# Kernel tuning notes

Hardware: AMD Instinct MI355X
Metric: run time of the kernel (lower is better)

Reference implementation:

```python
import jax, jax.numpy as jnp
import numpy as np

N = 50000      # nodes
E = 800000     # unique directed edges (avg degree 16)
F = 64         # input_dim
D = 64         # output_dim (== F -> residual is identity)
ALPHA = 0.5
LCS_THR = 0.5  # enable_lcs_masking=True, lcs_threshold=0.5


def setup_inputs() -> dict:
    key = jax.random.key(0)
    ks = jax.random.split(key, 16)
    x = jax.random.normal(ks[0], (N, F), jnp.float32)
    src = jax.random.randint(ks[1], (E,), 0, N, jnp.int32)
    dst = jax.random.randint(ks[2], (E,), 0, N, jnp.int32)
    # integer-valued multiplicities in {1,2,3,4} (recurring-transaction counts)
    counts = jnp.floor(jax.random.uniform(ks[3], (E,), jnp.float32) * 4.0) + 1.0
    def lin(k, fan_in, shape):
        return jax.random.normal(k, shape, jnp.float32) / np.float32(np.sqrt(fan_in))
    return dict(
        x=x, counts=counts,
        W_s2d=lin(ks[4], F, (F, D)), b_s2d=jnp.zeros((D,), jnp.float32),
        W_d2s=lin(ks[5], F, (F, D)), b_d2s=jnp.zeros((D,), jnp.float32),
        W_l1=lin(ks[6], 2 * F, (2 * F, F)), b_l1=jnp.zeros((F,), jnp.float32),
        W_l2=lin(ks[7], F, (F, 1)), b_l2=jnp.zeros((1,), jnp.float32),
        W_g1=lin(ks[8], 2 * D, (2 * D, D)), b_g1=jnp.zeros((D,), jnp.float32),
        W_g2=lin(ks[9], D, (D, 1)), b_g2=jnp.zeros((1,), jnp.float32),
        src=src, dst=dst,
    )


def reference(x, counts, W_s2d, b_s2d, W_d2s, b_d2s,
              W_l1, b_l1, W_l2, b_l2, W_g1, b_g1, W_g2, b_g2,
              src, dst):
    # in/out degrees from full (unmasked) multiplicities, clamped at 1
    in_deg = jnp.maximum(jax.ops.segment_sum(counts, dst, num_segments=N), 1.0)
    out_deg = jnp.maximum(jax.ops.segment_sum(counts, src, num_segments=N), 1.0)

    # LCS per unique edge: sigmoid(MLP([x_src, x_dst])), detached in torch
    lcs_in = jnp.concatenate([x[src], x[dst]], axis=-1)          # [E, 2F]
    lcs = jax.nn.sigmoid(
        jax.nn.relu(lcs_in @ W_l1 + b_l1) @ W_l2 + b_l2)[:, 0]   # [E]
    lcs = jax.lax.stop_gradient(lcs)
    keep = (lcs >= LCS_THR).astype(x.dtype)                      # LCS masking

    # symmetric-normalized edge weights with multiplicity counts
    w = counts * keep * jax.lax.rsqrt(out_deg[src] * in_deg[dst])  # [E]

    # direction-aware message passing (redundancy-eliminated, per unique edge)
    h_s2d = x @ W_s2d + b_s2d                                    # [N, D]
    h_d2s = x @ W_d2s + b_d2s                                    # [N, D]
    m_in = jax.ops.segment_sum(w[:, None] * h_s2d[src], dst, num_segments=N)
    m_out = jax.ops.segment_sum(w[:, None] * h_d2s[dst], src, num_segments=N)

    # node-wise gating over inbound vs outbound flows
    gate = jax.nn.sigmoid(
        jax.nn.relu(jnp.concatenate([m_in, m_out], axis=-1) @ W_g1 + b_g1)
        @ W_g2 + b_g2)                                           # [N, 1]

    # gated alpha-blend + identity residual (input_dim == output_dim)
    out = ALPHA * gate * m_in + (1.0 - ALPHA) * (1.0 - gate) * m_out + x
    return out
```

## Files before the change

kernel.cpp:

```cpp
#include <hip/hip_runtime.h>
#include <math.h>


typedef unsigned long long u64;
typedef unsigned short u16;

__device__ __forceinline__ float bflo(unsigned u) { return __uint_as_float(u << 16); }
__device__ __forceinline__ float bfhi(unsigned u) { return __uint_as_float(u & 0xffff0000u); }
__device__ __forceinline__ unsigned rne16(float f) {
    unsigned u = __float_as_uint(f);
    return (u + 0x7fffu + ((u >> 16) & 1u)) >> 16;
}

__global__ __launch_bounds__(256) void proj_zero_kernel(
    const float* __restrict__ x,
    const float* __restrict__ Wl1,  const float* __restrict__ bl1,
    const float* __restrict__ Ws2d, const float* __restrict__ bs2d,
    const float* __restrict__ Wd2s, const float* __restrict__ bd2s,
    float* __restrict__ A, float* __restrict__ B,
    unsigned* __restrict__ Ah, unsigned* __restrict__ Bh,
    unsigned* __restrict__ HSh, unsigned* __restrict__ HDh,
    int* __restrict__ zp, int nzero, int PB, int N)
{
    if (blockIdx.x >= PB) {
        const int t0 = (blockIdx.x - PB) * 256 + threadIdx.x;
        const int stride = (gridDim.x - PB) * 256;
        for (int i = t0; i < nzero; i += stride) zp[i] = 0;
        return;
    }
    __shared__ float xs[64][64];
    const int tid = threadIdx.x;
    const int n0  = blockIdx.x * 64;
    const int wv  = tid >> 6;
    const int cc  = tid & 63;

    const float* Wbase; const float* bias; float* obase; unsigned* obh;
    switch (wv) {
        case 0:  Wbase = Wl1;           bias = bl1;     obase = A;       obh = Ah;  break;
        case 1:  Wbase = Wl1 + 64 * 64; bias = nullptr; obase = B;       obh = Bh;  break;
        case 2:  Wbase = Ws2d;          bias = bs2d;    obase = nullptr; obh = HSh; break;
        default: Wbase = Wd2s;          bias = bd2s;    obase = nullptr; obh = HDh; break;
    }

    float wr[64];
#pragma unroll
    for (int k = 0; k < 64; ++k) wr[k] = Wbase[k * 64 + cc];
    const float bv = bias ? bias[cc] : 0.f;

#pragma unroll
    for (int j = 0; j < 4; ++j) {
        int f4  = tid + j * 256;
        int row = f4 >> 4;
        int c4  = f4 & 15;
        int gn  = n0 + row;
        float4 v = (gn < N) ? ((const float4*)x)[(long)gn * 16 + c4]
                            : make_float4(0.f, 0.f, 0.f, 0.f);
        ((float4*)&xs[row][0])[c4] = v;
    }
    __syncthreads();

    const int nmax = (N - n0 < 64) ? (N - n0) : 64;
    for (int n = 0; n < nmax; ++n) {
        float acc = bv;
#pragma unroll
        for (int k = 0; k < 64; k += 4) {
            float4 xv = *((const float4*)&xs[n][k]);
            acc += xv.x * wr[k] + xv.y * wr[k + 1] + xv.z * wr[k + 2] + xv.w * wr[k + 3];
        }
        if (obase) obase[(long)(n0 + n) * 64 + cc] = acc;
        const float part = __shfl_xor(acc, 1);
        if ((cc & 1) == 0)
            obh[(long)(n0 + n) * 32 + (cc >> 1)] = (rne16(part) << 16) | rne16(acc);
    }
}

#define LCS_MARGIN 0.04f
__global__ __launch_bounds__(256) void edge_w_kernel(
    const int* __restrict__ src, const int* __restrict__ dst,
    const float* __restrict__ counts,
    const float* __restrict__ A, const float* __restrict__ B,
    const unsigned* __restrict__ Ah, const unsigned* __restrict__ Bh,
    const float* __restrict__ Wl2, const float* __restrict__ bl2,
    u64* __restrict__ pk, unsigned* __restrict__ kslot, int N, int E)
{
    const int tid = threadIdx.x;
    const int e   = blockIdx.x * 16 + (tid >> 4);
    const int c   = tid & 15;
    if (e >= E) return;

    const int s = src[e];
    const int d = dst[e];
    const uint2 ua = *((const uint2*)(Ah + (long)s * 32 + c * 2));
    const uint2 ub = *((const uint2*)(Bh + (long)d * 32 + c * 2));
    const float4 wl = *((const float4*)(Wl2 + c * 4));

    float p = fmaxf(bflo(ua.x) + bflo(ub.x), 0.f) * wl.x
            + fmaxf(bfhi(ua.x) + bfhi(ub.x), 0.f) * wl.y
            + fmaxf(bflo(ua.y) + bflo(ub.y), 0.f) * wl.z
            + fmaxf(bfhi(ua.y) + bfhi(ub.y), 0.f) * wl.w;
    p += __shfl_xor(p, 1); p += __shfl_xor(p, 2);
    p += __shfl_xor(p, 4); p += __shfl_xor(p, 8);

    float z = p + bl2[0];
    if (fabsf(z) < LCS_MARGIN) {
        const float4 a = *((const float4*)(A + (long)s * 64 + c * 4));
        const float4 b = *((const float4*)(B + (long)d * 64 + c * 4));
        float q = fmaxf(a.x + b.x, 0.f) * wl.x + fmaxf(a.y + b.y, 0.f) * wl.y
                + fmaxf(a.z + b.z, 0.f) * wl.z + fmaxf(a.w + b.w, 0.f) * wl.w;
        q += __shfl_xor(q, 1); q += __shfl_xor(q, 2);
        q += __shfl_xor(q, 4); q += __shfl_xor(q, 8);
        z = q + bl2[0];
    }

    if (c == 0) {
        const u64 keep = (z >= 0.f) ? 1ull : 0ull;
        const u64 ic = (u64)(unsigned)__float2int_rn(counts[e]);
        const u64 od = atomicAdd(pk + d,     (keep << 32) | ic);
        const u64 os = atomicAdd(pk + N + s, (keep << 32) | ic);
        kslot[e] = keep ? ((((unsigned)(os >> 32)) << 16) | (unsigned)(od >> 32))
                        : 0xFFFFFFFFu;
    }
}

__global__ __launch_bounds__(256) void scan_reduce_kernel(
    const u64* __restrict__ pk, int* __restrict__ bsum, int M)
{
    __shared__ int sh[256];
    const int idx = blockIdx.x * 256 + threadIdx.x;
    sh[threadIdx.x] = (idx < M) ? (int)(pk[idx] >> 32) : 0;
    __syncthreads();
#pragma unroll
    for (int off = 128; off > 0; off >>= 1) {
        if (threadIdx.x < off) sh[threadIdx.x] += sh[threadIdx.x + off];
        __syncthreads();
    }
    if (threadIdx.x == 0) bsum[blockIdx.x] = sh[0];
}

__global__ __launch_bounds__(256) void scan_write_kernel(
    const u64* __restrict__ pk, const int* __restrict__ bsum,
    int* __restrict__ rp, int2* __restrict__ pkd, int2* __restrict__ pks,
    int M , int N, int NCH)
{
    __shared__ int s0[512], s1[512];
    const int tid = threadIdx.x;

    s0[tid]       = (tid < NCH)       ? bsum[tid]       : 0;
    s0[tid + 256] = (tid + 256 < NCH) ? bsum[tid + 256] : 0;
    __syncthreads();
    {
        int* cur = s0; int* nxt = s1;
        for (int off = 1; off < 512; off <<= 1) {
            nxt[tid]       = cur[tid]       + ((tid >= off)       ? cur[tid - off]       : 0);
            nxt[tid + 256] = cur[tid + 256] + ((tid + 256 >= off) ? cur[tid + 256 - off] : 0);
            __syncthreads();
            int* t = cur; cur = nxt; nxt = t;
        }
        if (tid == 0) s1[511] = 0;
        __syncthreads();
        if (cur != s0) { s0[tid] = cur[tid]; s0[tid + 256] = cur[tid + 256]; __syncthreads(); }
    }
    const int boff = (blockIdx.x == 0) ? 0 : s0[blockIdx.x - 1];
    __syncthreads();

    const int idx = blockIdx.x * 256 + tid;
    const u64 pv  = (idx < M) ? pk[idx] : 0ull;
    const int v   = (int)(pv >> 32);
    s0[tid] = v;
    __syncthreads();
    {
        int* cur = s0; int* nxt = s1;
        for (int off = 1; off < 256; off <<= 1) {
            nxt[tid] = cur[tid] + ((tid >= off) ? cur[tid - off] : 0);
            __syncthreads();
            int* t = cur; cur = nxt; nxt = t;
        }
        if (idx < M) {
            const int base = cur[tid] - v + boff;
            rp[idx] = base;
            const float isq = 1.f / sqrtf(fmaxf((float)(unsigned)pv, 1.f));
            if (idx < N) pkd[idx]     = make_int2(base, __float_as_int(isq));
            else         pks[idx - N] = make_int2(base, __float_as_int(isq));
            if (idx == M - 1) rp[M] = base + v;
        }
    }
}

__global__ __launch_bounds__(256) void place_kernel(
    const int* __restrict__ src, const int* __restrict__ dst,
    const float* __restrict__ counts, const unsigned* __restrict__ kslot,
    const int2* __restrict__ pkd, const int2* __restrict__ pks,
    unsigned* __restrict__ rec, int E)
{
    const int e = blockIdx.x * 256 + threadIdx.x;
    if (e >= E) return;
    const unsigned kk = kslot[e];
    if (kk == 0xFFFFFFFFu) return;
    const int s = src[e];
    const int d = dst[e];
    const int2 qd = pkd[d];
    const int2 qs = pks[s];
    const float w = counts[e] * __int_as_float(qd.y) * __int_as_float(qs.y);
    const unsigned wb = rne16(w);
    rec[qd.x + (int)(kk & 0xFFFFu)] = ((unsigned)s << 16) | wb;
    rec[qs.x + (int)(kk >> 16)]     = ((unsigned)d << 16) | wb;
}

__global__ __launch_bounds__(256) void gather_gate_kernel(
    const int* __restrict__ rp, const unsigned* __restrict__ rec,
    const unsigned* __restrict__ HSh, const unsigned* __restrict__ HDh,
    const float* __restrict__ x,
    const float* __restrict__ Wg1, const float* __restrict__ bg1,
    const float* __restrict__ Wg2, const float* __restrict__ bg2,
    float* __restrict__ out, int N)
{
    __shared__ float mbuf[4][128];
    const int tid  = threadIdx.x;
    const int wv   = tid >> 6;
    const int lane = tid & 63;
    const int g    = lane >> 3;
    const int c    = lane & 7;
    const int n    = blockIdx.x * 4 + wv;
    if (n >= N) return;

    float mi[8], mo[8];
#pragma unroll
    for (int j = 0; j < 8; ++j) { mi[j] = 0.f; mo[j] = 0.f; }

    {
        const int end = rp[n + 1];
        int i = rp[n] + g;
        for (; i + 8 < end; i += 16) {
            const unsigned ra = rec[i];
            const unsigned rb = rec[i + 8];
            const float wa = bflo(ra), wb = bflo(rb);
            const uint4 ua = *((const uint4*)(HSh + (long)(ra >> 16) * 32 + c * 4));
            const uint4 ub = *((const uint4*)(HSh + (long)(rb >> 16) * 32 + c * 4));
            mi[0] += wa * bflo(ua.x) + wb * bflo(ub.x);
            mi[1] += wa * bfhi(ua.x) + wb * bfhi(ub.x);
            mi[2] += wa * bflo(ua.y) + wb * bflo(ub.y);
            mi[3] += wa * bfhi(ua.y) + wb * bfhi(ub.y);
            mi[4] += wa * bflo(ua.z) + wb * bflo(ub.z);
            mi[5] += wa * bfhi(ua.z) + wb * bfhi(ub.z);
            mi[6] += wa * bflo(ua.w) + wb * bflo(ub.w);
            mi[7] += wa * bfhi(ua.w) + wb * bfhi(ub.w);
        }
        if (i < end) {
            const unsigned ra = rec[i];
            const float wa = bflo(ra);
            const uint4 ua = *((const uint4*)(HSh + (long)(ra >> 16) * 32 + c * 4));
            mi[0] += wa * bflo(ua.x); mi[1] += wa * bfhi(ua.x);
            mi[2] += wa * bflo(ua.y); mi[3] += wa * bfhi(ua.y);
            mi[4] += wa * bflo(ua.z); mi[5] += wa * bfhi(ua.z);
            mi[6] += wa * bflo(ua.w); mi[7] += wa * bfhi(ua.w);
        }
    }
    {
        const int end = rp[N + n + 1];
        int i = rp[N + n] + g;
        for (; i + 8 < end; i += 16) {
            const unsigned ra = rec[i];
            const unsigned rb = rec[i + 8];
            const float wa = bflo(ra), wb = bflo(rb);
            const uint4 ua = *((const uint4*)(HDh + (long)(ra >> 16) * 32 + c * 4));
            const uint4 ub = *((const uint4*)(HDh + (long)(rb >> 16) * 32 + c * 4));
            mo[0] += wa * bflo(ua.x) + wb * bflo(ub.x);
            mo[1] += wa * bfhi(ua.x) + wb * bfhi(ub.x);
            mo[2] += wa * bflo(ua.y) + wb * bflo(ub.y);
            mo[3] += wa * bfhi(ua.y) + wb * bfhi(ub.y);
            mo[4] += wa * bflo(ua.z) + wb * bflo(ub.z);
            mo[5] += wa * bfhi(ua.z) + wb * bfhi(ub.z);
            mo[6] += wa * bflo(ua.w) + wb * bflo(ub.w);
            mo[7] += wa * bfhi(ua.w) + wb * bfhi(ub.w);
        }
        if (i < end) {
            const unsigned ra = rec[i];
            const float wa = bflo(ra);
            const uint4 ua = *((const uint4*)(HDh + (long)(ra >> 16) * 32 + c * 4));
            mo[0] += wa * bflo(ua.x); mo[1] += wa * bfhi(ua.x);
            mo[2] += wa * bflo(ua.y); mo[3] += wa * bfhi(ua.y);
            mo[4] += wa * bflo(ua.z); mo[5] += wa * bfhi(ua.z);
            mo[6] += wa * bflo(ua.w); mo[7] += wa * bfhi(ua.w);
        }
    }

#pragma unroll
    for (int j = 0; j < 8; ++j) {
        mi[j] += __shfl_xor(mi[j], 8);
        mi[j] += __shfl_xor(mi[j], 16);
        mi[j] += __shfl_xor(mi[j], 32);
        mo[j] += __shfl_xor(mo[j], 8);
        mo[j] += __shfl_xor(mo[j], 16);
        mo[j] += __shfl_xor(mo[j], 32);
    }
    if (g == 0) {
#pragma unroll
        for (int j = 0; j < 8; ++j) {
            mbuf[wv][c * 8 + j]      = mi[j];
            mbuf[wv][64 + c * 8 + j] = mo[j];
        }
    }

    float acc = bg1[lane];
    const float* mb = &mbuf[wv][0];
#pragma unroll 8
    for (int k4 = 0; k4 < 32; ++k4) {
        const float4 m4 = ((const float4*)mb)[k4];
        const int k = k4 * 4;
        acc += m4.x * Wg1[(k + 0) * 64 + lane] + m4.y * Wg1[(k + 1) * 64 + lane]
             + m4.z * Wg1[(k + 2) * 64 + lane] + m4.w * Wg1[(k + 3) * 64 + lane];
    }
    float v = fmaxf(acc, 0.f) * Wg2[lane];
    v += __shfl_xor(v, 1);  v += __shfl_xor(v, 2);  v += __shfl_xor(v, 4);
    v += __shfl_xor(v, 8);  v += __shfl_xor(v, 16); v += __shfl_xor(v, 32);

    const float gate = 1.f / (1.f + expf(-(v + bg2[0])));
    const float miv = mb[lane];
    const float mov = mb[64 + lane];
    out[(long)n * 64 + lane] = 0.5f * gate * miv + 0.5f * (1.f - gate) * mov
                             + x[(long)n * 64 + lane];
}

extern "C" void kernel_launch(void* const* d_in, const int* in_sizes, int n_in,
                              void* d_out, int out_size, void* d_ws, size_t ws_size,
                              hipStream_t stream) {
    const float* x      = (const float*)d_in[0];
    const float* counts = (const float*)d_in[1];
    const float* Ws2d   = (const float*)d_in[2];
    const float* bs2d   = (const float*)d_in[3];
    const float* Wd2s   = (const float*)d_in[4];
    const float* bd2s   = (const float*)d_in[5];
    const float* Wl1    = (const float*)d_in[6];
    const float* bl1    = (const float*)d_in[7];
    const float* Wl2    = (const float*)d_in[8];
    const float* bl2    = (const float*)d_in[9];
    const float* Wg1    = (const float*)d_in[10];
    const float* bg1    = (const float*)d_in[11];
    const float* Wg2    = (const float*)d_in[12];
    const float* bg2    = (const float*)d_in[13];
    const int*   src    = (const int*)d_in[14];
    const int*   dst    = (const int*)d_in[15];

    const int N   = in_sizes[0] / 64;
    const int E   = in_sizes[14];
    const int M   = 2 * N;
    const int NCH = (M + 255) / 256;
    const int PB  = (N + 63) / 64;

    float* ws      = (float*)d_ws;
    float* A       = ws;
    float* B       = A + 64L * N;
    unsigned* Ah   = (unsigned*)(B + 64L * N);
    unsigned* Bh   = Ah + 32L * N;
    unsigned* HSh  = Bh + 32L * N;
    unsigned* HDh  = HSh + 32L * N;
    u64* pk        = (u64*)(HDh + 32L * N);
    int* bsum      = (int*)(pk + M);
    int* rp        = bsum + 512;
    int2* pkd      = (int2*)(rp + M + 2);
    int2* pks      = pkd + N;
    unsigned* kslot = (unsigned*)(pks + N);
    unsigned* rec   = kslot + (long)E;

    proj_zero_kernel<<<PB + 64, 256, 0, stream>>>(
        x, Wl1, bl1, Ws2d, bs2d, Wd2s, bd2s, A, B, Ah, Bh, HSh, HDh,
        (int*)pk, 4 * N, PB, N);

    edge_w_kernel<<<(E + 15) / 16, 256, 0, stream>>>(
        src, dst, counts, A, B, Ah, Bh, Wl2, bl2, pk, kslot, N, E);

    scan_reduce_kernel<<<NCH, 256, 0, stream>>>(pk, bsum, M);

    scan_write_kernel<<<NCH, 256, 0, stream>>>(pk, bsum, rp, pkd, pks, M, N, NCH);

    place_kernel<<<(E + 255) / 256, 256, 0, stream>>>(
        src, dst, counts, kslot, pkd, pks, rec, E);

    gather_gate_kernel<<<(N + 3) / 4, 256, 0, stream>>>(
        rp, rec, HSh, HDh, x, Wg1, bg1, Wg2, bg2, (float*)d_out, N);
}
```

Baseline: 293.4 us.

## Widen edge LCS loads to 8 lanes per edge and repack gate weights as float4

The edge scoring kernel now uses 8 lanes per edge with 16-byte loads instead of 16 lanes with 8-byte loads. That halves the shuffle reduction steps and doubles the edges handled per block. An extra block in the projection kernel rearranges Wg1 into a float4-interleaved layout, so the gate MLP in the gather kernel issues one vector load per four weights. An unneeded shared-memory write and barrier in the scan are also removed. The cost is an extra workspace region that shifts every other buffer, plus a small extra block in the first launch.

```diff
diff --git a/kernel.cpp b/kernel.cpp
--- a/kernel.cpp
+++ b/kernel.cpp
@@ -17,14 +17,22 @@
     const float* __restrict__ Wl1,  const float* __restrict__ bl1,
     const float* __restrict__ Ws2d, const float* __restrict__ bs2d,
     const float* __restrict__ Wd2s, const float* __restrict__ bd2s,
+    const float* __restrict__ Wg1,  float* __restrict__ Wg1q,
     float* __restrict__ A, float* __restrict__ B,
     unsigned* __restrict__ Ah, unsigned* __restrict__ Bh,
     unsigned* __restrict__ HSh, unsigned* __restrict__ HDh,
     int* __restrict__ zp, int nzero, int PB, int N)
 {
     if (blockIdx.x >= PB) {
+        if (blockIdx.x == PB + 64) {
+            for (int i = threadIdx.x; i < 8192; i += 256) {
+                const int k = i >> 6, c = i & 63;
+                Wg1q[((k >> 2) * 64 + c) * 4 + (k & 3)] = Wg1[i];
+            }
+            return;
+        }
         const int t0 = (blockIdx.x - PB) * 256 + threadIdx.x;
-        const int stride = (gridDim.x - PB) * 256;
+        const int stride = 64 * 256;
         for (int i = t0; i < nzero; i += stride) zp[i] = 0;
         return;
     }
@@ -84,31 +92,38 @@
     u64* __restrict__ pk, unsigned* __restrict__ kslot, int N, int E)
 {
     const int tid = threadIdx.x;
-    const int e   = blockIdx.x * 16 + (tid >> 4);
-    const int c   = tid & 15;
+    const int e   = blockIdx.x * 32 + (tid >> 3);
+    const int c   = tid & 7;
     if (e >= E) return;
 
     const int s = src[e];
     const int d = dst[e];
-    const uint2 ua = *((const uint2*)(Ah + (long)s * 32 + c * 2));
-    const uint2 ub = *((const uint2*)(Bh + (long)d * 32 + c * 2));
-    const float4 wl = *((const float4*)(Wl2 + c * 4));
-
-    float p = fmaxf(bflo(ua.x) + bflo(ub.x), 0.f) * wl.x
-            + fmaxf(bfhi(ua.x) + bfhi(ub.x), 0.f) * wl.y
-            + fmaxf(bflo(ua.y) + bflo(ub.y), 0.f) * wl.z
-            + fmaxf(bfhi(ua.y) + bfhi(ub.y), 0.f) * wl.w;
-    p += __shfl_xor(p, 1); p += __shfl_xor(p, 2);
-    p += __shfl_xor(p, 4); p += __shfl_xor(p, 8);
+    const uint4  ua  = *((const uint4*)(Ah + (long)s * 32 + c * 4));
+    const uint4  ub  = *((const uint4*)(Bh + (long)d * 32 + c * 4));
+    const float4 wl0 = *((const float4*)(Wl2 + c * 8));
+    const float4 wl1 = *((const float4*)(Wl2 + c * 8 + 4));
+
+    float p = fmaxf(bflo(ua.x) + bflo(ub.x), 0.f) * wl0.x
+            + fmaxf(bfhi(ua.x) + bfhi(ub.x), 0.f) * wl0.y
+            + fmaxf(bflo(ua.y) + bflo(ub.y), 0.f) * wl0.z
+            + fmaxf(bfhi(ua.y) + bfhi(ub.y), 0.f) * wl0.w
+            + fmaxf(bflo(ua.z) + bflo(ub.z), 0.f) * wl1.x
+            + fmaxf(bfhi(ua.z) + bfhi(ub.z), 0.f) * wl1.y
+            + fmaxf(bflo(ua.w) + bflo(ub.w), 0.f) * wl1.z
+            + fmaxf(bfhi(ua.w) + bfhi(ub.w), 0.f) * wl1.w;
+    p += __shfl_xor(p, 1); p += __shfl_xor(p, 2); p += __shfl_xor(p, 4);
 
     float z = p + bl2[0];
     if (fabsf(z) < LCS_MARGIN) {
-        const float4 a = *((const float4*)(A + (long)s * 64 + c * 4));
-        const float4 b = *((const float4*)(B + (long)d * 64 + c * 4));
-        float q = fmaxf(a.x + b.x, 0.f) * wl.x + fmaxf(a.y + b.y, 0.f) * wl.y
-                + fmaxf(a.z + b.z, 0.f) * wl.z + fmaxf(a.w + b.w, 0.f) * wl.w;
-        q += __shfl_xor(q, 1); q += __shfl_xor(q, 2);
-        q += __shfl_xor(q, 4); q += __shfl_xor(q, 8);
+        const float4 a0 = *((const float4*)(A + (long)s * 64 + c * 8));
+        const float4 a1 = *((const float4*)(A + (long)s * 64 + c * 8 + 4));
+        const float4 b0 = *((const float4*)(B + (long)d * 64 + c * 8));
+        const float4 b1 = *((const float4*)(B + (long)d * 64 + c * 8 + 4));
+        float q = fmaxf(a0.x + b0.x, 0.f) * wl0.x + fmaxf(a0.y + b0.y, 0.f) * wl0.y
+                + fmaxf(a0.z + b0.z, 0.f) * wl0.z + fmaxf(a0.w + b0.w, 0.f) * wl0.w
+                + fmaxf(a1.x + b1.x, 0.f) * wl1.x + fmaxf(a1.y + b1.y, 0.f) * wl1.y
+                + fmaxf(a1.z + b1.z, 0.f) * wl1.z + fmaxf(a1.w + b1.w, 0.f) * wl1.w;
+        q += __shfl_xor(q, 1); q += __shfl_xor(q, 2); q += __shfl_xor(q, 4);
         z = q + bl2[0];
     }
 
@@ -156,8 +171,6 @@
             __syncthreads();
             int* t = cur; cur = nxt; nxt = t;
         }
-        if (tid == 0) s1[511] = 0;
-        __syncthreads();
         if (cur != s0) { s0[tid] = cur[tid]; s0[tid + 256] = cur[tid + 256]; __syncthreads(); }
     }
     const int boff = (blockIdx.x == 0) ? 0 : s0[blockIdx.x - 1];
@@ -210,7 +223,7 @@
     const int* __restrict__ rp, const unsigned* __restrict__ rec,
     const unsigned* __restrict__ HSh, const unsigned* __restrict__ HDh,
     const float* __restrict__ x,
-    const float* __restrict__ Wg1, const float* __restrict__ bg1,
+    const float* __restrict__ Wg1q, const float* __restrict__ bg1,
     const float* __restrict__ Wg2, const float* __restrict__ bg2,
     float* __restrict__ out, int N)
 {
@@ -306,9 +319,8 @@
 #pragma unroll 8
     for (int k4 = 0; k4 < 32; ++k4) {
         const float4 m4 = ((const float4*)mb)[k4];
-        const int k = k4 * 4;
-        acc += m4.x * Wg1[(k + 0) * 64 + lane] + m4.y * Wg1[(k + 1) * 64 + lane]
-             + m4.z * Wg1[(k + 2) * 64 + lane] + m4.w * Wg1[(k + 3) * 64 + lane];
+        const float4 w4 = ((const float4*)Wg1q)[k4 * 64 + lane];
+        acc += m4.x * w4.x + m4.y * w4.y + m4.z * w4.z + m4.w * w4.w;
     }
     float v = fmaxf(acc, 0.f) * Wg2[lane];
     v += __shfl_xor(v, 1);  v += __shfl_xor(v, 2);  v += __shfl_xor(v, 4);
@@ -348,7 +360,8 @@
     const int PB  = (N + 63) / 64;
 
     float* ws      = (float*)d_ws;
-    float* A       = ws;
+    float* Wg1q    = ws;
+    float* A       = ws + 8192;
     float* B       = A + 64L * N;
     unsigned* Ah   = (unsigned*)(B + 64L * N);
     unsigned* Bh   = Ah + 32L * N;
@@ -362,11 +375,11 @@
     unsigned* kslot = (unsigned*)(pks + N);
     unsigned* rec   = kslot + (long)E;
 
-    proj_zero_kernel<<<PB + 64, 256, 0, stream>>>(
-        x, Wl1, bl1, Ws2d, bs2d, Wd2s, bd2s, A, B, Ah, Bh, HSh, HDh,
-        (int*)pk, 4 * N, PB, N);
-
-    edge_w_kernel<<<(E + 15) / 16, 256, 0, stream>>>(
+    proj_zero_kernel<<<PB + 65, 256, 0, stream>>>(
+        x, Wl1, bl1, Ws2d, bs2d, Wd2s, bd2s, Wg1, Wg1q,
+        A, B, Ah, Bh, HSh, HDh, (int*)pk, 4 * N, PB, N);
+
+    edge_w_kernel<<<(E + 31) / 32, 256, 0, stream>>>(
         src, dst, counts, A, B, Ah, Bh, Wl2, bl2, pk, kslot, N, E);
 
     scan_reduce_kernel<<<NCH, 256, 0, stream>>>(pk, bsum, M);
@@ -377,5 +390,5 @@
         src, dst, counts, kslot, pkd, pks, rec, E);
 
     gather_gate_kernel<<<(N + 3) / 4, 256, 0, stream>>>(
-        rp, rec, HSh, HDh, x, Wg1, bg1, Wg2, bg2, (float*)d_out, N);
-}
+        rp, rec, HSh, HDh, x, Wg1q, bg1, Wg2, bg2, (float*)d_out, N);
+}
```

Result: no change. 293.3 us (-0.0%).
